# Kernel optimization log

Measured on AMD Instinct MI355X. Metric: run time of the kernel, lower is better.

## Reference

```python
import jax, jax.numpy as jnp
import numpy as np


def setup_inputs() -> dict:
    key = jax.random.key(0)
    k1, k2 = jax.random.split(key)
    B, C, H, W = 1, 128, 96, 128
    feat_l = jax.random.normal(k1, (B, C, H, W), dtype=jnp.float32)
    feat_r = jax.random.normal(k2, (B, C, H, W), dtype=jnp.float32)
    return {"feat_l": feat_l, "feat_r": feat_r, "scale_x": 4, "scale_y": 4}


def reference(feat_l, feat_r, scale_x, scale_y):
    B, C, H, W = feat_l.shape
    _, _, H_R, W_R = feat_r.shape
    # Full correlation volume: [B, H, W, H_R*W_R]  (the huge intermediate)
    corr = jnp.einsum('bchw,bcij->bhwij', feat_l, feat_r).reshape(B, H, W, H_R * W_R)
    flow_cost = jnp.max(corr, axis=3)           # [B, H, W]
    flat_idx = jnp.argmax(corr, axis=3)         # [B, H, W] int
    # Decode argmax index -> flow (u, v) relative to pixel grid
    xoff = jnp.arange(W)                        # [W]
    yoff = jnp.arange(H)                        # [H]
    u = -((flat_idx % W_R) * scale_x - xoff[None, None, :]).astype(jnp.float32)
    v = -((flat_idx // W_R) * scale_y - yoff[None, :, None]).astype(jnp.float32)
    flow = jnp.stack([u, v], axis=3)            # [B, H, W, 2]
    return flow, flow_cost
```

## Files before the change

kernel.cpp:

```cpp
#include <hip/hip_runtime.h>

#define K_TOT 128
#define H_DIM 96
#define W_DIM 128
#define M_TOT (H_DIM * W_DIM)
#define N_TOT (H_DIM * W_DIM)
#define SCALE 4
#define NEG_INF (-3.402823e38f)

#define KP 384
#define NH 24
#define SLAB_F16 24576

typedef _Float16 f16x8 __attribute__((ext_vector_type(8)));
typedef float f32x16 __attribute__((ext_vector_type(16)));

__global__ __launch_bounds__(256)
void split_prep_kernel(const float* __restrict__ L, const float* __restrict__ R,
                       _Float16* __restrict__ Ls, _Float16* __restrict__ Rs,
                       unsigned long long* __restrict__ keys) {
    const int t = threadIdx.x;
    if (blockIdx.x >= 384) {
        int m = (blockIdx.x - 384) * 256 + t;
        if (m < M_TOT) keys[m] = 0ull;
        return;
    }
    __shared__ __align__(16) _Float16 T[3][64][144];
    const int isR  = blockIdx.x >= 192;
    const int slab = blockIdx.x - (isR ? 192 : 0);
    const int P0   = slab * 64;
    const float* src = isR ? R : L;
    _Float16* dst = isR ? Rs : Ls;

    const int p4 = (t & 15) * 4;
    const int k0 = t >> 4;
#pragma unroll
    for (int it = 0; it < 8; ++it) {
        const int k = k0 + it * 16;
        float4 v = *(const float4*)&src[(size_t)k * M_TOT + P0 + p4];
        float xs[4] = {v.x, v.y, v.z, v.w};
#pragma unroll
        for (int j = 0; j < 4; ++j) {
            _Float16 h = (_Float16)xs[j];
            float hf = (float)h;
            float r = xs[j] - hf;
            T[0][p4 + j][k] = h;
            T[1][p4 + j][k] = (_Float16)(r * 64.0f);
            T[2][p4 + j][k] = (_Float16)(hf * 0.015625f);
        }
    }
    __syncthreads();
#pragma unroll
    for (int it = 0; it < 12; ++it) {
        const int c    = it * 256 + t;
        const int col  = c & 31;
        const int hi   = (c >> 5) & 1;
        const int op   = (c >> 6) & 1;
        const int half = c >> 7;
        const int sec  = half >> 3;
        const int kb   = (half & 7) * 16 + hi * 8;
        const int plane = (sec == 0) ? 0 : (isR ? sec : 3 - sec);
        const int row  = op * 32 + col;
        float4 v = *(const float4*)&T[plane][row][kb];
        *(float4*)&dst[(size_t)slab * SLAB_F16 + (size_t)c * 8] = v;
    }
}

__global__ __launch_bounds__(256, 4)
void mfma_corr_kernel(const _Float16* __restrict__ Ls, const _Float16* __restrict__ Rs,
                      unsigned long long* __restrict__ keys) {
    __shared__ float vals[128 * 17];
    __shared__ int   idxs[128 * 17];

    const int tid  = threadIdx.x;
    const int lane = tid & 63;
    const int wid  = tid >> 6;
    const int wr   = wid >> 1;
    const int wc   = wid & 1;
    const int col  = lane & 31;
    const int hi   = lane >> 5;
    const int bid  = blockIdx.x;
    const int xcd  = bid & 7;
    const int b    = bid >> 3;
    const int mt   = b / 12;
    const int nt   = xcd * 12 + b % 12;
    const int m0   = mt * 128;
    const int n0   = nt * 128;

    const _Float16* pA = Ls + (size_t)(mt * 2 + wr) * SLAB_F16 + lane * 8;
    const _Float16* pB = Rs + (size_t)(nt * 2 + wc) * SLAB_F16 + lane * 8;

    f32x16 acc[2][2];
#pragma unroll
    for (int mi = 0; mi < 2; ++mi)
#pragma unroll
        for (int ni = 0; ni < 2; ++ni) acc[mi][ni] = (f32x16)(0.0f);

    f16x8 fA[3][2], fB[3][2];
#define LOADH(hh, s) {                                              \
        fA[s][0] = *(const f16x8*)(pA + (hh) * 1024);               \
        fA[s][1] = *(const f16x8*)(pA + (hh) * 1024 + 512);         \
        fB[s][0] = *(const f16x8*)(pB + (hh) * 1024);               \
        fB[s][1] = *(const f16x8*)(pB + (hh) * 1024 + 512);         \
    }
    LOADH(0, 0);
    LOADH(1, 1);
#pragma unroll
    for (int h = 0; h < NH; ++h) {
        if (h + 2 < NH) LOADH(h + 2, (h + 2) % 3);
        const int s = h % 3;
        __builtin_amdgcn_s_setprio(1);
        acc[0][0] = __builtin_amdgcn_mfma_f32_32x32x16_f16(fA[s][0], fB[s][0], acc[0][0], 0, 0, 0);
        acc[0][1] = __builtin_amdgcn_mfma_f32_32x32x16_f16(fA[s][0], fB[s][1], acc[0][1], 0, 0, 0);
        acc[1][0] = __builtin_amdgcn_mfma_f32_32x32x16_f16(fA[s][1], fB[s][0], acc[1][0], 0, 0, 0);
        acc[1][1] = __builtin_amdgcn_mfma_f32_32x32x16_f16(fA[s][1], fB[s][1], acc[1][1], 0, 0, 0);
        __builtin_amdgcn_s_setprio(0);
    }
#undef LOADH

#pragma unroll
    for (int mi = 0; mi < 2; ++mi) {
#pragma unroll
        for (int reg = 0; reg < 16; ++reg) {
            float best = acc[mi][0][reg];
            int bni = 0;
            if (acc[mi][1][reg] > best) { best = acc[mi][1][reg]; bni = 1; }
            int n = n0 + wc * 64 + bni * 32 + col;
#pragma unroll
            for (int d = 16; d >= 8; d >>= 1) {
                float ov = __shfl_xor(best, d, 64);
                int   oi = __shfl_xor(n, d, 64);
                if (ov > best || (ov == best && oi < n)) { best = ov; n = oi; }
            }
            if ((lane & 24) == 0) {
                const int row = wr * 64 + mi * 32 + (reg & 3) + 8 * (reg >> 2) + 4 * hi;
                const int c   = wc * 8 + (lane & 7);
                vals[row * 17 + c] = best;
                idxs[row * 17 + c] = n;
            }
        }
    }
    __syncthreads();
    if (tid < 128) {
        float bv = vals[tid * 17 + 0]; int bi = idxs[tid * 17 + 0];
#pragma unroll
        for (int c = 1; c < 16; ++c) {
            float v = vals[tid * 17 + c]; int ix = idxs[tid * 17 + c];
            if (v > bv || (v == bv && ix < bi)) { bv = v; bi = ix; }
        }
        unsigned vb = __float_as_uint(bv);
        vb = (vb & 0x80000000u) ? ~vb : (vb | 0x80000000u);
        unsigned long long key = ((unsigned long long)vb << 32) | (unsigned)(~bi);
        atomicMax(&keys[m0 + tid], key);
    }
}

__global__ void finalize_keys_kernel(const unsigned long long* __restrict__ keys,
                                     float* __restrict__ out) {
    int m = blockIdx.x * blockDim.x + threadIdx.x;
    if (m >= M_TOT) return;
    unsigned long long key = keys[m];
    unsigned hi = (unsigned)(key >> 32);
    unsigned bits = (hi & 0x80000000u) ? (hi & 0x7fffffffu) : ~hi;
    float v = __uint_as_float(bits);
    int idx = (int)(~(unsigned)(key & 0xffffffffu));
    int h = m / W_DIM, w = m % W_DIM;
    int i = idx / W_DIM, j = idx % W_DIM;
    out[m * 2 + 0] = (float)(w - SCALE * j);
    out[m * 2 + 1] = (float)(h - SCALE * i);
    out[2 * M_TOT + m] = v;
}

#define BM 128
#define BN 128
#define KB 32
__global__ __launch_bounds__(256)
void corr_argmax_kernel(const float* __restrict__ L, const float* __restrict__ R,
                        float* __restrict__ pbest, int* __restrict__ pidx,
                        int nsplit) {
    __shared__ float As[KB][BM];
    __shared__ float Bs[KB][BN];
    const int tid = threadIdx.x;
    const int mtiles = M_TOT / BM;
    const int mt = blockIdx.x % mtiles;
    const int s  = blockIdx.x / mtiles;
    const int m0 = mt * BM;
    const int ns = N_TOT / nsplit;
    const int ntiles = ns / BN;
    const int tx = tid & 15;
    const int ty = tid >> 4;
    float rbest[8]; int ridx[8];
#pragma unroll
    for (int i = 0; i < 8; ++i) { rbest[i] = NEG_INF; ridx[i] = 0; }
    for (int nt = 0; nt < ntiles; ++nt) {
        const int n0 = s * ns + nt * BN;
        float acc[8][8];
#pragma unroll
        for (int i = 0; i < 8; ++i)
#pragma unroll
            for (int j = 0; j < 8; ++j) acc[i][j] = 0.f;
        for (int kb = 0; kb < K_TOT; kb += KB) {
            __syncthreads();
#pragma unroll
            for (int r = 0; r < 4; ++r) {
                int f  = tid + 256 * r;
                int kk = f >> 5;
                int c4 = f & 31;
                float4 va = *reinterpret_cast<const float4*>(&L[(size_t)(kb + kk) * M_TOT + m0 + c4 * 4]);
                *reinterpret_cast<float4*>(&As[kk][c4 * 4]) = va;
                float4 vb = *reinterpret_cast<const float4*>(&R[(size_t)(kb + kk) * N_TOT + n0 + c4 * 4]);
                *reinterpret_cast<float4*>(&Bs[kk][c4 * 4]) = vb;
            }
            __syncthreads();
#pragma unroll 4
            for (int kk = 0; kk < KB; ++kk) {
                float4 a0 = *reinterpret_cast<const float4*>(&As[kk][ty * 4]);
                float4 a1 = *reinterpret_cast<const float4*>(&As[kk][64 + ty * 4]);
                float4 b0 = *reinterpret_cast<const float4*>(&Bs[kk][tx * 4]);
                float4 b1 = *reinterpret_cast<const float4*>(&Bs[kk][64 + tx * 4]);
                float a[8] = {a0.x, a0.y, a0.z, a0.w, a1.x, a1.y, a1.z, a1.w};
                float b[8] = {b0.x, b0.y, b0.z, b0.w, b1.x, b1.y, b1.z, b1.w};
#pragma unroll
                for (int i = 0; i < 8; ++i)
#pragma unroll
                    for (int j = 0; j < 8; ++j)
                        acc[i][j] = fmaf(a[i], b[j], acc[i][j]);
            }
        }
#pragma unroll
        for (int i = 0; i < 8; ++i)
#pragma unroll
            for (int jh = 0; jh < 2; ++jh)
#pragma unroll
                for (int jj = 0; jj < 4; ++jj) {
                    int n = n0 + jh * 64 + tx * 4 + jj;
                    float v = acc[i][jh * 4 + jj];
                    if (v > rbest[i]) { rbest[i] = v; ridx[i] = n; }
                }
    }
    __syncthreads();
    float (*redv)[BM] = reinterpret_cast<float(*)[BM]>(&As[0][0]);
    int   (*redi)[BM] = reinterpret_cast<int  (*)[BM]>(&Bs[0][0]);
#pragma unroll
    for (int i = 0; i < 8; ++i) {
        int row = (i >> 2) * 64 + ty * 4 + (i & 3);
        redv[tx][row] = rbest[i];
        redi[tx][row] = ridx[i];
    }
    __syncthreads();
    if (tid < BM) {
        float bv = NEG_INF; int bi = 0x7fffffff;
        for (int t = 0; t < 16; ++t) {
            float v  = redv[t][tid];
            int   ix = redi[t][tid];
            if (v > bv || (v == bv && ix < bi)) { bv = v; bi = ix; }
        }
        pbest[(size_t)s * M_TOT + m0 + tid] = bv;
        pidx [(size_t)s * M_TOT + m0 + tid] = bi;
    }
}

__global__ void finalize_parts_kernel(const float* __restrict__ pbest,
                                      const int* __restrict__ pidx,
                                      float* __restrict__ out, int nsplit) {
    int m = blockIdx.x * blockDim.x + threadIdx.x;
    if (m >= M_TOT) return;
    float bv = NEG_INF; int bi = 0x7fffffff;
    for (int s = 0; s < nsplit; ++s) {
        float v  = pbest[(size_t)s * M_TOT + m];
        int   ix = pidx [(size_t)s * M_TOT + m];
        if (v > bv || (v == bv && ix < bi)) { bv = v; bi = ix; }
    }
    int h = m / W_DIM, w = m % W_DIM;
    int i = bi / W_DIM, j = bi % W_DIM;
    out[m * 2 + 0] = (float)(w - SCALE * j);
    out[m * 2 + 1] = (float)(h - SCALE * i);
    out[2 * M_TOT + m] = bv;
}

extern "C" void kernel_launch(void* const* d_in, const int* in_sizes, int n_in,
                              void* d_out, int out_size, void* d_ws, size_t ws_size,
                              hipStream_t stream) {
    const float* L = (const float*)d_in[0];
    const float* R = (const float*)d_in[1];
    float* out = (float*)d_out;

    const size_t PKbytes = (size_t)M_TOT * KP * sizeof(_Float16);
    const size_t need = 2 * PKbytes + (size_t)M_TOT * 8;
    if (ws_size >= need) {
        _Float16* Ls = (_Float16*)d_ws;
        _Float16* Rs = (_Float16*)((char*)d_ws + PKbytes);
        unsigned long long* keys = (unsigned long long*)((char*)d_ws + 2 * PKbytes);
        split_prep_kernel<<<dim3(432), dim3(256), 0, stream>>>(L, R, Ls, Rs, keys);
        mfma_corr_kernel<<<dim3((M_TOT / 128) * (N_TOT / 128)), dim3(256), 0, stream>>>(Ls, Rs, keys);
        finalize_keys_kernel<<<dim3(48), dim3(256), 0, stream>>>(keys, out);
    } else {
        int nsplit = 8;
        while (nsplit > 1 && (size_t)nsplit * M_TOT * 8 > ws_size) nsplit >>= 1;
        float* pbest = (float*)d_ws;
        int*   pidx  = (int*)((char*)d_ws + (size_t)nsplit * M_TOT * sizeof(float));
        corr_argmax_kernel<<<dim3((M_TOT / BM) * nsplit), dim3(256), 0, stream>>>(L, R, pbest, pidx, nsplit);
        finalize_parts_kernel<<<dim3((M_TOT + 255) / 256), dim3(256), 0, stream>>>(pbest, pidx, out, nsplit);
    }
}
```

Baseline: 235.6 us.

## Split K across two wave groups in MFMA correlation kernel with LDS reduction

The block grows to 512 threads so two groups of four waves each compute half of the K dimension (12 of 24 steps), then partial accumulators are summed through shared memory before the argmax epilogue. The aim is more waves in flight and a shorter per-wave serial MFMA chain, hiding global load latency. In exchange it adds a 64KB shared buffer, two extra barriers and an LDS exchange, which limit how many blocks fit per CU.

```diff
diff --git a/kernel.cpp b/kernel.cpp
--- a/kernel.cpp
+++ b/kernel.cpp
@@ -10,6 +10,7 @@
 
 #define KP 384
 #define NH 24
+#define NH2 12
 #define SLAB_F16 24576
 
 typedef _Float16 f16x8 __attribute__((ext_vector_type(8)));
@@ -66,17 +67,18 @@
     }
 }
 
-__global__ __launch_bounds__(256, 4)
+__global__ __launch_bounds__(512, 4)
 void mfma_corr_kernel(const _Float16* __restrict__ Ls, const _Float16* __restrict__ Rs,
                       unsigned long long* __restrict__ keys) {
-    __shared__ float vals[128 * 17];
-    __shared__ int   idxs[128 * 17];
+    __shared__ __align__(16) char smem[65536];
 
     const int tid  = threadIdx.x;
     const int lane = tid & 63;
     const int wid  = tid >> 6;
-    const int wr   = wid >> 1;
-    const int wc   = wid & 1;
+    const int kh   = wid >> 2;
+    const int sw   = wid & 3;
+    const int wr   = sw >> 1;
+    const int wc   = sw & 1;
     const int col  = lane & 31;
     const int hi   = lane >> 5;
     const int bid  = blockIdx.x;
@@ -87,8 +89,8 @@
     const int m0   = mt * 128;
     const int n0   = nt * 128;
 
-    const _Float16* pA = Ls + (size_t)(mt * 2 + wr) * SLAB_F16 + lane * 8;
-    const _Float16* pB = Rs + (size_t)(nt * 2 + wc) * SLAB_F16 + lane * 8;
+    const _Float16* pA = Ls + (size_t)(mt * 2 + wr) * SLAB_F16 + kh * (NH2 * 1024) + lane * 8;
+    const _Float16* pB = Rs + (size_t)(nt * 2 + wc) * SLAB_F16 + kh * (NH2 * 1024) + lane * 8;
 
     f32x16 acc[2][2];
 #pragma unroll
@@ -106,8 +108,8 @@
     LOADH(0, 0);
     LOADH(1, 1);
 #pragma unroll
-    for (int h = 0; h < NH; ++h) {
-        if (h + 2 < NH) LOADH(h + 2, (h + 2) % 3);
+    for (int h = 0; h < NH2; ++h) {
+        if (h + 2 < NH2) LOADH(h + 2, (h + 2) % 3);
         const int s = h % 3;
         __builtin_amdgcn_s_setprio(1);
         acc[0][0] = __builtin_amdgcn_mfma_f32_32x32x16_f16(fA[s][0], fB[s][0], acc[0][0], 0, 0, 0);
@@ -118,25 +120,64 @@
     }
 #undef LOADH
 
-#pragma unroll
-    for (int mi = 0; mi < 2; ++mi) {
-#pragma unroll
-        for (int reg = 0; reg < 16; ++reg) {
-            float best = acc[mi][0][reg];
-            int bni = 0;
-            if (acc[mi][1][reg] > best) { best = acc[mi][1][reg]; bni = 1; }
-            int n = n0 + wc * 64 + bni * 32 + col;
-#pragma unroll
-            for (int d = 16; d >= 8; d >>= 1) {
-                float ov = __shfl_xor(best, d, 64);
-                int   oi = __shfl_xor(n, d, 64);
-                if (ov > best || (ov == best && oi < n)) { best = ov; n = oi; }
-            }
-            if ((lane & 24) == 0) {
-                const int row = wr * 64 + mi * 32 + (reg & 3) + 8 * (reg >> 2) + 4 * hi;
-                const int c   = wc * 8 + (lane & 7);
-                vals[row * 17 + c] = best;
-                idxs[row * 17 + c] = n;
+    if (kh == 1) {
+        float* ex = (float*)smem + sw * 4096;
+#pragma unroll
+        for (int mi = 0; mi < 2; ++mi)
+#pragma unroll
+            for (int ni = 0; ni < 2; ++ni) {
+                const int frag = mi * 2 + ni;
+#pragma unroll
+                for (int q = 0; q < 4; ++q) {
+                    float4 v = { acc[mi][ni][q * 4 + 0], acc[mi][ni][q * 4 + 1],
+                                 acc[mi][ni][q * 4 + 2], acc[mi][ni][q * 4 + 3] };
+                    *(float4*)&ex[frag * 1024 + q * 256 + lane * 4] = v;
+                }
+            }
+    }
+    __syncthreads();
+    if (kh == 0) {
+        const float* ex = (const float*)smem + sw * 4096;
+#pragma unroll
+        for (int mi = 0; mi < 2; ++mi)
+#pragma unroll
+            for (int ni = 0; ni < 2; ++ni) {
+                const int frag = mi * 2 + ni;
+#pragma unroll
+                for (int q = 0; q < 4; ++q) {
+                    float4 v = *(const float4*)&ex[frag * 1024 + q * 256 + lane * 4];
+                    acc[mi][ni][q * 4 + 0] += v.x;
+                    acc[mi][ni][q * 4 + 1] += v.y;
+                    acc[mi][ni][q * 4 + 2] += v.z;
+                    acc[mi][ni][q * 4 + 3] += v.w;
+                }
+            }
+    }
+    __syncthreads();
+
+    float* vals = (float*)smem;
+    int*   idxs = (int*)(smem + 8704);
+    if (kh == 0) {
+#pragma unroll
+        for (int mi = 0; mi < 2; ++mi) {
+#pragma unroll
+            for (int reg = 0; reg < 16; ++reg) {
+                float best = acc[mi][0][reg];
+                int bni = 0;
+                if (acc[mi][1][reg] > best) { best = acc[mi][1][reg]; bni = 1; }
+                int n = n0 + wc * 64 + bni * 32 + col;
+#pragma unroll
+                for (int d = 16; d >= 8; d >>= 1) {
+                    float ov = __shfl_xor(best, d, 64);
+                    int   oi = __shfl_xor(n, d, 64);
+                    if (ov > best || (ov == best && oi < n)) { best = ov; n = oi; }
+                }
+                if ((lane & 24) == 0) {
+                    const int row = wr * 64 + mi * 32 + (reg & 3) + 8 * (reg >> 2) + 4 * hi;
+                    const int c   = wc * 8 + (lane & 7);
+                    vals[row * 17 + c] = best;
+                    idxs[row * 17 + c] = n;
+                }
             }
         }
     }
@@ -292,7 +333,7 @@
         _Float16* Rs = (_Float16*)((char*)d_ws + PKbytes);
         unsigned long long* keys = (unsigned long long*)((char*)d_ws + 2 * PKbytes);
         split_prep_kernel<<<dim3(432), dim3(256), 0, stream>>>(L, R, Ls, Rs, keys);
-        mfma_corr_kernel<<<dim3((M_TOT / 128) * (N_TOT / 128)), dim3(256), 0, stream>>>(Ls, Rs, keys);
+        mfma_corr_kernel<<<dim3((M_TOT / 128) * (N_TOT / 128)), dim3(512), 0, stream>>>(Ls, Rs, keys);
         finalize_keys_kernel<<<dim3(48), dim3(256), 0, stream>>>(keys, out);
     } else {
         int nsplit = 8;
```

Result: slower. 340.4 us (+44.5%).
